# Kernel tuning notes

Hardware: AMD Instinct MI355X
Metric: run time of the kernel (lower is better)

The kernel has to match this reference:

```python
import jax, jax.numpy as jnp
import numpy as np

B = 65536
L = 128          # latent_dim
H = 20           # hidden_size of first LSTMCell
H2 = 2           # hidden_size of projection LSTMCell
NEG_SLOPE = 0.01 # F.leaky_relu default


def _uniform(k, shape, bound):
    return jax.random.uniform(k, shape, jnp.float32, -bound, bound)


def setup_inputs() -> dict:
    key = jax.random.key(0)
    ks = jax.random.split(key, 12)
    b1 = 1.0 / np.sqrt(H)
    b2 = 1.0 / np.sqrt(H2)
    return {
        "mu": jax.random.normal(ks[0], (B, L), jnp.float32),
        "log_var": jax.random.normal(ks[1], (B, L), jnp.float32),
        "eps0": jax.random.normal(ks[2], (B,), jnp.float32),
        "eps": jax.random.normal(ks[3], (L, B), jnp.float32),
        # lstm_unit: input_size=2, hidden=20 -> gates 4H
        "Wih1": _uniform(ks[4], (4 * H, 2), b1),
        "Whh1": _uniform(ks[5], (4 * H, H), b1),
        "bih1": _uniform(ks[6], (4 * H,), b1),
        "bhh1": _uniform(ks[7], (4 * H,), b1),
        # lstm_projection: input_size=2H, hidden=2 -> gates 4*2
        "Wih2": _uniform(ks[8], (4 * H2, 2 * H), b2),
        "Whh2": _uniform(ks[9], (4 * H2, H2), b2),
        "bih2": _uniform(ks[10], (4 * H2,), b2),
        "bhh2": _uniform(ks[11], (4 * H2,), b2),
    }


def _lstm_cell(x, h, c, Wih, Whh, bih, bhh):
    # torch.nn.LSTMCell: gates ordered i, f, g, o
    g = x @ Wih.T + h @ Whh.T + (bih + bhh)
    i, f, gg, o = jnp.split(g, 4, axis=1)
    c_new = jax.nn.sigmoid(f) * c + jax.nn.sigmoid(i) * jnp.tanh(gg)
    h_new = jax.nn.sigmoid(o) * jnp.tanh(c_new)
    return h_new, c_new


def reference(mu, log_var, eps0, eps,
              Wih1, Whh1, bih1, bhh1,
              Wih2, Whh2, bih2, bhh2):
    b = mu.shape[0]
    latent_dim = mu.shape[1]

    # initial reparameterized input from dim 0
    x0 = eps0 * jnp.exp(0.5 * log_var[:, 0]) + mu[:, 0]
    inp0 = jnp.stack([x0, jnp.zeros_like(x0)], axis=1)  # [B, 2]

    carry0 = (
        jnp.zeros((b, H), mu.dtype),   # hidden_state
        jnp.zeros((b, H), mu.dtype),   # cell_state
        jnp.zeros((b, H2), mu.dtype),  # hidden_state_second
        jnp.zeros((b, H2), mu.dtype),  # cell_state_second
        inp0,                          # current input [B, 2]
    )
    xs = (eps, mu.T, jnp.arange(latent_dim, dtype=mu.dtype))  # per-step [B], [B], []

    def step(carry, xs_t):
        h1, c1, h2, c2, x = carry
        eps_t, mu_t, idx = xs_t
        h1, c1 = _lstm_cell(x, h1, c1, Wih1, Whh1, bih1, bhh1)
        out1 = jax.nn.leaky_relu(jnp.concatenate([h1, c1], axis=1), NEG_SLOPE)
        h2, c2 = _lstm_cell(out1, h2, c2, Wih2, Whh2, bih2, bhh2)
        mu_r = h2[:, 0]
        lv_r = h2[:, 1]
        samp = eps_t * jnp.exp(0.5 * lv_r) + mu_r
        # sample=False: teacher-force next input from mu[:, idx]
        nxt = jnp.stack([mu_t, jnp.full_like(mu_t, 0.0) + idx], axis=1)
        return (h1, c1, h2, c2, nxt), (mu_r, lv_r, samp)

    _, (mus_r, lvs_r, samples) = jax.lax.scan(step, carry0, xs)
    # [L, B] -> [B, L]
    return mus_r.T, lvs_r.T, samples.T
```

## Files before the change

kernel.cpp:

```cpp
#include <hip/hip_runtime.h>

#define BB 65536
#define LL 128
#define HH 20
#define LOG2E 1.4426950408889634f

typedef __attribute__((ext_vector_type(8))) short  bf16x8;
typedef __attribute__((ext_vector_type(4))) float  f32x4;
typedef __attribute__((ext_vector_type(2))) float  f32x2;
typedef __attribute__((ext_vector_type(4))) int    i32x4;

__device__ __forceinline__ float frcp(float x)  { return __builtin_amdgcn_rcpf(x); }
__device__ __forceinline__ float ex2(float x)   { return __builtin_amdgcn_exp2f(x); }
__device__ __forceinline__ float lrelu(float x) { return fmaxf(x, 0.01f * x); }
__device__ __forceinline__ float csign(float mag, float sgn) {
    int m = __builtin_bit_cast(int, mag), s = __builtin_bit_cast(int, sgn);
    return __builtin_bit_cast(float, (m & 0x7fffffff) | (s & 0x80000000));
}
__device__ __forceinline__ unsigned cvt_pk(float lo, float hi) {
    unsigned r;
    asm("v_cvt_pk_bf16_f32 %0, %1, %2" : "=v"(r) : "v"(lo), "v"(hi));
    return r;
}
__device__ __forceinline__ bf16x8 pack8v(f32x4 a, f32x4 b) {
    i32x4 t = { (int)cvt_pk(a[0], a[1]), (int)cvt_pk(a[2], a[3]),
                (int)cvt_pk(b[0], b[1]), (int)cvt_pk(b[2], b[3]) };
    return __builtin_bit_cast(bf16x8, t);
}

__device__ __forceinline__ void lstm_unit(f32x4 a, float& c, float& h) {
    float ei  = ex2(-a[0]);
    float ef  = ex2(-a[1]);
    float eo  = ex2(-a[3]);
    float egm = ex2(-fabsf(a[2] + a[2]));
    float numg = 1.f - egm, deng = 1.f + egm;
    float A = 1.f + ef, B = 1.f + ei;
    float P = B * deng;
    float D = P * A;
    float n2 = csign(numg * A, a[2]);
    float cn = fmaf(c, P, n2) * frcp(D);
    c = cn;
    float ecm = ex2(-fabsf(cn * (2.f * LOG2E)));
    float numc = 1.f - ecm;
    float Do = (1.f + eo) * (1.f + ecm);
    h = csign(numc, cn) * frcp(Do);
}

__device__ __forceinline__ void lstm_unit2(f32x4 a0, f32x4 a1, f32x2& c, f32x2& h) {
    f32x2 gg = {a0[2], a1[2]};
    f32x2 ei  = {ex2(-a0[0]), ex2(-a1[0])};
    f32x2 ef  = {ex2(-a0[1]), ex2(-a1[1])};
    f32x2 eo  = {ex2(-a0[3]), ex2(-a1[3])};
    f32x2 tg  = gg + gg;
    f32x2 egm = {ex2(-fabsf(tg[0])), ex2(-fabsf(tg[1]))};
    f32x2 numg = 1.f - egm;
    f32x2 deng = 1.f + egm;
    f32x2 A = 1.f + ef, B = 1.f + ei;
    f32x2 P = B * deng;
    f32x2 D = P * A;
    f32x2 nA = numg * A;
    f32x2 n2 = {csign(nA[0], gg[0]), csign(nA[1], gg[1])};
    f32x2 rD = {frcp(D[0]), frcp(D[1])};
    f32x2 cn = (c * P + n2) * rD;
    c = cn;
    f32x2 tc = cn * (2.f * LOG2E);
    f32x2 ecm = {ex2(-fabsf(tc[0])), ex2(-fabsf(tc[1]))};
    f32x2 numc = 1.f - ecm;
    f32x2 Do = (1.f + eo) * (1.f + ecm);
    f32x2 rDo = {frcp(Do[0]), frcp(Do[1])};
    f32x2 sc = {csign(numc[0], cn[0]), csign(numc[1], cn[1])};
    h = sc * rDo;
}

__global__ __launch_bounds__(256) void sampler_lstm(
    const float* __restrict__ mu, const float* __restrict__ log_var,
    const float* __restrict__ eps0, const float* __restrict__ eps,
    const float* __restrict__ Wih1, const float* __restrict__ Whh1,
    const float* __restrict__ bih1, const float* __restrict__ bhh1,
    const float* __restrict__ Wih2, const float* __restrict__ Whh2,
    const float* __restrict__ bih2, const float* __restrict__ bhh2,
    float* __restrict__ out)
{
    __shared__ __align__(16) float ob[4][3][16][20];

    const int tid  = threadIdx.x;
    const int wave = tid >> 6;
    const int lane = tid & 63;
    const int b16  = lane & 15;
    const int q    = lane >> 4;
    const int gb0  = (blockIdx.x * 4 + wave) * 16;
    const int gb   = gb0 + b16;

    float (*obw)[16][20] = ob[wave];

    bf16x8 a1[5];
    #pragma unroll
    for (int T = 0; T < 5; ++T) {
        int G = 16 * T + b16;
        int j = G >> 2, g = G & 3;
        int row = g * HH + j;
        float v[8];
        #pragma unroll
        for (int e = 0; e < 8; ++e) {
            float val = 0.f;
            if (e < 4)        val = Whh1[row * HH + 4 * e + q];
            else if (e == 4)  val = Whh1[row * HH + 16 + q];
            else if (q == 0) {
                if (e == 5)      val = Wih1[row * 2 + 0];
                else if (e == 6) val = Wih1[row * 2 + 1];
                else             val = bih1[row] + bhh1[row];
            }
            v[e] = val * LOG2E;
        }
        f32x4 lo = {v[0], v[1], v[2], v[3]}, hi4 = {v[4], v[5], v[6], v[7]};
        a1[T] = pack8v(lo, hi4);
    }
    bf16x8 a2f[2];
    #pragma unroll
    for (int f = 0; f < 2; ++f) {
        float v[8];
        #pragma unroll
        for (int e = 0; e < 8; ++e) {
            float val = 0.f;
            if (b16 < 8) {
                int u = b16 >> 2, p = b16 & 3;
                int ro = 2 * p + u;
                if (f == 0) {
                    if (e < 4)       val = Wih2[ro * 40 + 4 * e + q];
                    else if (e == 4) val = Wih2[ro * 40 + 16 + q];
                } else {
                    if (e < 4)       val = Wih2[ro * 40 + 20 + 4 * e + q];
                    else if (e == 4) val = Wih2[ro * 40 + 36 + q];
                    else if (q == 0) {
                        if (e == 5)      val = Whh2[ro * 2 + 0];
                        else if (e == 6) val = Whh2[ro * 2 + 1];
                        else             val = bih2[ro] + bhh2[ro];
                    }
                }
            }
            v[e] = val * LOG2E;
        }
        f32x4 lo = {v[0], v[1], v[2], v[3]}, hi4 = {v[4], v[5], v[6], v[7]};
        a2f[f] = pack8v(lo, hi4);
    }

    const float* murow = mu + (size_t)gb * LL;
    float samp0 = eps0[gb] * ex2(0.5f * LOG2E * log_var[(size_t)gb * LL]) + murow[0];

    const f32x4 kz = {0.f, 0.f, 0.f, 0.f};
    f32x2 c01 = {0.f, 0.f}, c23 = {0.f, 0.f};
    float c4 = 0.f, c2 = 0.f;
    float xA = (q == 0) ? samp0 : 0.f;
    float xB = 0.f;
    float h2self = 0.f, h2oth = 0.f;

    const float* epsp = eps + gb;

    f32x4 zlo = {0.f, 0.f, 0.f, 0.f};
    f32x4 phi = {0.f, xA, xB, 1.f};
    bf16x8 b1 = pack8v(zlo, phi);

    #pragma unroll 1
    for (int tb = 0; tb < 8; ++tb) {
        #pragma unroll 2
        for (int ti = 0; ti < 16; ++ti) {
            const int t = tb * 16 + ti;
            float ldmu = 0.f, ldeps = 0.f;
            if (q == 0) { ldmu = murow[t]; ldeps = *epsp; }
            epsp += BB;

            f32x4 acc[5];
            #pragma unroll
            for (int T = 0; T < 5; ++T)
                acc[T] = __builtin_amdgcn_mfma_f32_16x16x32_bf16(a1[T], b1, kz, 0, 0, 0);

            f32x2 h01, h23;
            float h4;
            lstm_unit2(acc[0], acc[1], c01, h01);
            lstm_unit2(acc[2], acc[3], c23, h23);
            lstm_unit(acc[4], c4, h4);

            f32x4 hv = {h01[0], h01[1], h23[0], h23[1]};
            f32x4 cv = {c01[0], c01[1], c23[0], c23[1]};
            f32x4 b1hi = {h4, ldmu, (float)t, 1.f};
            b1 = pack8v(hv, b1hi);

            f32x4 l0 = {lrelu(hv[0]), lrelu(hv[1]), lrelu(hv[2]), lrelu(hv[3])};
            f32x4 l1 = {lrelu(h4), 0.f, 0.f, 0.f};
            f32x4 l2 = {lrelu(cv[0]), lrelu(cv[1]), lrelu(cv[2]), lrelu(cv[3])};
            f32x4 l3 = {lrelu(c4), h2self, h2oth, 1.f};
            bf16x8 b2a = pack8v(l0, l1);
            bf16x8 b2b = pack8v(l2, l3);

            f32x4 g2 = __builtin_amdgcn_mfma_f32_16x16x32_bf16(a2f[0], b2a, kz, 0, 0, 0);
            g2 = __builtin_amdgcn_mfma_f32_16x16x32_bf16(a2f[1], b2b, g2, 0, 0, 0);

            float h2;
            lstm_unit(g2, c2, h2);
            h2self = h2;
            h2oth  = __shfl_xor(h2, 16);

            if (q == 0) {
                obw[0][b16][ti] = h2;
                obw[1][b16][ti] = h2oth;
                obw[2][b16][ti] = fmaf(ldeps, ex2(0.5f * LOG2E * h2oth), h2);
            }
        }

        {
            int bq = lane >> 2, ch = lane & 3;
            #pragma unroll
            for (int o = 0; o < 3; ++o) {
                f32x4 v = *reinterpret_cast<const f32x4*>(&obw[o][bq][ch * 4]);
                float* dst = out + (size_t)o * BB * LL + (size_t)(gb0 + bq) * LL
                           + tb * 16 + ch * 4;
                *(float4*)dst = make_float4(v[0], v[1], v[2], v[3]);
            }
        }
    }
}

extern "C" void kernel_launch(void* const* d_in, const int* in_sizes, int n_in,
                              void* d_out, int out_size, void* d_ws, size_t ws_size,
                              hipStream_t stream) {
    sampler_lstm<<<dim3(BB / 64), dim3(256), 0, stream>>>(
        (const float*)d_in[0],  (const float*)d_in[1],  (const float*)d_in[2],
        (const float*)d_in[3],  (const float*)d_in[4],  (const float*)d_in[5],
        (const float*)d_in[6],  (const float*)d_in[7],  (const float*)d_in[8],
        (const float*)d_in[9],  (const float*)d_in[10], (const float*)d_in[11],
        (float*)d_out);
}
```

Before: 237.9 us.

## Software-pipeline second LSTM cell one step behind and pair it with first

Restructures the time loop so each step's projection-cell activation is deferred into the next iteration. There it is computed together with the fifth first-cell unit in a paired lstm_unit2 call. This shortens the serial dependency chain per step and lets the MFMA for the next step overlap with the second-cell math. It adds a prologue and epilogue, and the output flush is now indexed by a shifted slot, which adds some control-flow complexity.

```diff
diff --git a/kernel.cpp b/kernel.cpp
--- a/kernel.cpp
+++ b/kernel.cpp
@@ -150,72 +150,117 @@
     const f32x4 kz = {0.f, 0.f, 0.f, 0.f};
     f32x2 c01 = {0.f, 0.f}, c23 = {0.f, 0.f};
     float c4 = 0.f, c2 = 0.f;
-    float xA = (q == 0) ? samp0 : 0.f;
-    float xB = 0.f;
     float h2self = 0.f, h2oth = 0.f;
-
     const float* epsp = eps + gb;
 
-    f32x4 zlo = {0.f, 0.f, 0.f, 0.f};
-    f32x4 phi = {0.f, xA, xB, 1.f};
-    bf16x8 b1 = pack8v(zlo, phi);
-
-    #pragma unroll 1
-    for (int tb = 0; tb < 8; ++tb) {
-        #pragma unroll 2
-        for (int ti = 0; ti < 16; ++ti) {
-            const int t = tb * 16 + ti;
-            float ldmu = 0.f, ldeps = 0.f;
-            if (q == 0) { ldmu = murow[t]; ldeps = *epsp; }
-            epsp += BB;
-
-            f32x4 acc[5];
-            #pragma unroll
-            for (int T = 0; T < 5; ++T)
-                acc[T] = __builtin_amdgcn_mfma_f32_16x16x32_bf16(a1[T], b1, kz, 0, 0, 0);
-
-            f32x2 h01, h23;
-            float h4;
-            lstm_unit2(acc[0], acc[1], c01, h01);
-            lstm_unit2(acc[2], acc[3], c23, h23);
-            lstm_unit(acc[4], c4, h4);
-
-            f32x4 hv = {h01[0], h01[1], h23[0], h23[1]};
-            f32x4 cv = {c01[0], c01[1], c23[0], c23[1]};
-            f32x4 b1hi = {h4, ldmu, (float)t, 1.f};
-            b1 = pack8v(hv, b1hi);
-
-            f32x4 l0 = {lrelu(hv[0]), lrelu(hv[1]), lrelu(hv[2]), lrelu(hv[3])};
-            f32x4 l1 = {lrelu(h4), 0.f, 0.f, 0.f};
-            f32x4 l2 = {lrelu(cv[0]), lrelu(cv[1]), lrelu(cv[2]), lrelu(cv[3])};
-            f32x4 l3 = {lrelu(c4), h2self, h2oth, 1.f};
-            bf16x8 b2a = pack8v(l0, l1);
-            bf16x8 b2b = pack8v(l2, l3);
-
-            f32x4 g2 = __builtin_amdgcn_mfma_f32_16x16x32_bf16(a2f[0], b2a, kz, 0, 0, 0);
-            g2 = __builtin_amdgcn_mfma_f32_16x16x32_bf16(a2f[1], b2b, g2, 0, 0, 0);
-
-            float h2;
-            lstm_unit(g2, c2, h2);
-            h2self = h2;
-            h2oth  = __shfl_xor(h2, 16);
-
-            if (q == 0) {
-                obw[0][b16][ti] = h2;
-                obw[1][b16][ti] = h2oth;
-                obw[2][b16][ti] = fmaf(ldeps, ex2(0.5f * LOG2E * h2oth), h2);
-            }
-        }
-
-        {
+    bf16x8 b1;
+    f32x4 g2s;
+    float epsv;
+
+    {
+        float ldmu = 0.f, ldeps = 0.f;
+        if (q == 0) { ldmu = murow[0]; ldeps = *epsp; }
+        epsp += BB;
+
+        f32x4 zlo = {0.f, 0.f, 0.f, 0.f};
+        f32x4 phi = {0.f, (q == 0) ? samp0 : 0.f, 0.f, 1.f};
+        bf16x8 b1p = pack8v(zlo, phi);
+
+        f32x4 acc[5];
+        #pragma unroll
+        for (int T = 0; T < 5; ++T)
+            acc[T] = __builtin_amdgcn_mfma_f32_16x16x32_bf16(a1[T], b1p, kz, 0, 0, 0);
+
+        f32x2 h01, h23;
+        float h4;
+        lstm_unit2(acc[0], acc[1], c01, h01);
+        lstm_unit2(acc[2], acc[3], c23, h23);
+        lstm_unit(acc[4], c4, h4);
+
+        f32x4 hv = {h01[0], h01[1], h23[0], h23[1]};
+        f32x4 cv = {c01[0], c01[1], c23[0], c23[1]};
+        f32x4 b1hi = {h4, ldmu, 0.f, 1.f};
+        b1 = pack8v(hv, b1hi);
+
+        f32x4 l0 = {lrelu(hv[0]), lrelu(hv[1]), lrelu(hv[2]), lrelu(hv[3])};
+        f32x4 l1 = {lrelu(h4), 0.f, 0.f, 0.f};
+        f32x4 l2 = {lrelu(cv[0]), lrelu(cv[1]), lrelu(cv[2]), lrelu(cv[3])};
+        f32x4 l3 = {lrelu(c4), h2self, h2oth, 1.f};
+        g2s = __builtin_amdgcn_mfma_f32_16x16x32_bf16(a2f[0], pack8v(l0, l1), kz, 0, 0, 0);
+        g2s = __builtin_amdgcn_mfma_f32_16x16x32_bf16(a2f[1], pack8v(l2, l3), g2s, 0, 0, 0);
+        epsv = ldeps;
+    }
+
+    #pragma unroll 2
+    for (int t = 1; t < LL; ++t) {
+        float ldmu = 0.f, ldeps = 0.f;
+        if (q == 0) { ldmu = murow[t]; ldeps = *epsp; }
+        epsp += BB;
+
+        f32x4 acc[5];
+        #pragma unroll
+        for (int T = 0; T < 5; ++T)
+            acc[T] = __builtin_amdgcn_mfma_f32_16x16x32_bf16(a1[T], b1, kz, 0, 0, 0);
+
+        f32x2 h01, h23;
+        lstm_unit2(acc[0], acc[1], c01, h01);
+        lstm_unit2(acc[2], acc[3], c23, h23);
+        f32x2 c42 = {c4, c2}, h42;
+        lstm_unit2(acc[4], g2s, c42, h42);
+        c4 = c42[0];  c2 = c42[1];
+        float h4 = h42[0];
+        h2self = h42[1];
+        h2oth  = __shfl_xor(h2self, 16);
+
+        if (q == 0) {
+            int s = (t - 1) & 15;
+            obw[0][b16][s] = h2self;
+            obw[1][b16][s] = h2oth;
+            obw[2][b16][s] = fmaf(epsv, ex2(0.5f * LOG2E * h2oth), h2self);
+        }
+
+        f32x4 hv = {h01[0], h01[1], h23[0], h23[1]};
+        f32x4 cv = {c01[0], c01[1], c23[0], c23[1]};
+        f32x4 b1hi = {h4, ldmu, (float)t, 1.f};
+        b1 = pack8v(hv, b1hi);
+
+        f32x4 l0 = {lrelu(hv[0]), lrelu(hv[1]), lrelu(hv[2]), lrelu(hv[3])};
+        f32x4 l1 = {lrelu(h4), 0.f, 0.f, 0.f};
+        f32x4 l2 = {lrelu(cv[0]), lrelu(cv[1]), lrelu(cv[2]), lrelu(cv[3])};
+        f32x4 l3 = {lrelu(c4), h2self, h2oth, 1.f};
+        g2s = __builtin_amdgcn_mfma_f32_16x16x32_bf16(a2f[0], pack8v(l0, l1), kz, 0, 0, 0);
+        g2s = __builtin_amdgcn_mfma_f32_16x16x32_bf16(a2f[1], pack8v(l2, l3), g2s, 0, 0, 0);
+        epsv = ldeps;
+
+        if ((t & 15) == 0) {
+            int bk = (t >> 4) - 1;
             int bq = lane >> 2, ch = lane & 3;
             #pragma unroll
             for (int o = 0; o < 3; ++o) {
                 f32x4 v = *reinterpret_cast<const f32x4*>(&obw[o][bq][ch * 4]);
                 float* dst = out + (size_t)o * BB * LL + (size_t)(gb0 + bq) * LL
-                           + tb * 16 + ch * 4;
+                           + bk * 16 + ch * 4;
                 *(float4*)dst = make_float4(v[0], v[1], v[2], v[3]);
             }
+        }
+    }
+
+    {
+        float h2;
+        lstm_unit(g2s, c2, h2);
+        float h2o = __shfl_xor(h2, 16);
+        if (q == 0) {
+            obw[0][b16][15] = h2;
+            obw[1][b16][15] = h2o;
+            obw[2][b16][15] = fmaf(epsv, ex2(0.5f * LOG2E * h2o), h2);
+        }
+        int bq = lane >> 2, ch = lane & 3;
+        #pragma unroll
+        for (int o = 0; o < 3; ++o) {
+            f32x4 v = *reinterpret_cast<const f32x4*>(&obw[o][bq][ch * 4]);
+            float* dst = out + (size_t)o * BB * LL + (size_t)(gb0 + bq) * LL
+                       + 7 * 16 + ch * 4;
+            *(float4*)dst = make_float4(v[0], v[1], v[2], v[3]);
         }
     }
 }
```

New measurement: 236.6 us. No clear change (-0.5%).
